# Kernel optimization log

Hardware: AMD Instinct MI355X
Metric: run time of the kernel (lower is better)

## Reference

```python
import jax, jax.numpy as jnp
import numpy as np

C_S, C_P, C_H, H, P_QK, P_V = 384, 128, 16, 12, 4, 8
B, N = 1, 512
INF = 1e5
EPS = 1e-8


def quat_to_rot(q):
    w, x, y, z = q[..., 0], q[..., 1], q[..., 2], q[..., 3]
    return jnp.stack([
        jnp.stack([1 - 2 * (y * y + z * z), 2 * (x * y - w * z), 2 * (x * z + w * y)], -1),
        jnp.stack([2 * (x * y + w * z), 1 - 2 * (x * x + z * z), 2 * (y * z - w * x)], -1),
        jnp.stack([2 * (x * z - w * y), 2 * (y * z + w * x), 1 - 2 * (x * x + y * y)], -1),
    ], -2)


def layer_norm(x, g, b):
    m = x.mean(-1, keepdims=True)
    v = ((x - m) ** 2).mean(-1, keepdims=True)
    return (x - m) * jax.lax.rsqrt(v + 1e-5) * g + b


def setup_inputs():
    key = jax.random.key(0)
    ks = iter(jax.random.split(key, 64))

    def w(shape, scale=0.02):
        return jax.random.normal(next(ks), shape, dtype=jnp.float32) * scale

    inp = {}
    inp['s'] = jax.random.normal(next(ks), (B, N, C_S), dtype=jnp.float32)
    inp['p'] = jax.random.normal(next(ks), (B, N, N, C_P), dtype=jnp.float32)
    q = jax.random.normal(next(ks), (B, N, 4), dtype=jnp.float32)
    inp['rot'] = quat_to_rot(q / jnp.linalg.norm(q, axis=-1, keepdims=True))
    inp['trans'] = jax.random.normal(next(ks), (B, N, 3), dtype=jnp.float32)
    inp['mask'] = jnp.ones((B, N), dtype=jnp.float32)
    inp['w_q'] = w((C_S, H * C_H)); inp['b_q'] = jnp.zeros((H * C_H,), jnp.float32)
    inp['w_kv'] = w((C_S, 2 * H * C_H)); inp['b_kv'] = jnp.zeros((2 * H * C_H,), jnp.float32)
    inp['w_qp'] = w((C_S, H * P_QK * 3)); inp['b_qp'] = jnp.zeros((H * P_QK * 3,), jnp.float32)
    inp['w_kvp'] = w((C_S, H * (P_QK + P_V) * 3)); inp['b_kvp'] = jnp.zeros((H * (P_QK + P_V) * 3,), jnp.float32)
    inp['w_b'] = w((C_P, H)); inp['b_b'] = jnp.zeros((H,), jnp.float32)
    inp['head_w'] = w((H,), 0.5)
    d_out = H * (C_H + C_P + P_V * 4)  # 2112
    inp['w_o'] = w((d_out, C_S)); inp['b_o'] = jnp.zeros((C_S,), jnp.float32)
    inp['ln1_g'] = jnp.ones((C_S,), jnp.float32); inp['ln1_b'] = jnp.zeros((C_S,), jnp.float32)
    for i in (1, 2, 3):
        inp['tw%d' % i] = w((C_S, C_S)); inp['tb%d' % i] = jnp.zeros((C_S,), jnp.float32)
    inp['ln2_g'] = jnp.ones((C_S,), jnp.float32); inp['ln2_b'] = jnp.zeros((C_S,), jnp.float32)
    inp['bb_w'] = w((C_S, 6)); inp['bb_b'] = jnp.zeros((6,), jnp.float32)
    return inp


def forward(s, p, rot, trans, mask, w_q, b_q, w_kv, b_kv, w_qp, b_qp, w_kvp, b_kvp,
            w_b, b_b, head_w, w_o, b_o, ln1_g, ln1_b,
            tw1, tb1, tw2, tb2, tw3, tb3, ln2_g, ln2_b, bb_w, bb_b):
    # ---- Invariant Point Attention ----
    q = (s @ w_q + b_q).reshape(B, N, H, C_H)
    k, v = jnp.split((s @ w_kv + b_kv).reshape(B, N, H, 2 * C_H), 2, axis=-1)
    qp = (s @ w_qp + b_qp).reshape(B, N, H * P_QK, 3)
    qp = (jnp.einsum('bnij,bnpj->bnpi', rot, qp) + trans[:, :, None, :]).reshape(B, N, H, P_QK, 3)
    kvp = (s @ w_kvp + b_kvp).reshape(B, N, H * (P_QK + P_V), 3)
    kvp = (jnp.einsum('bnij,bnpj->bnpi', rot, kvp) + trans[:, :, None, :]).reshape(B, N, H, P_QK + P_V, 3)
    kp, vp = kvp[..., :P_QK, :], kvp[..., P_QK:, :]
    bias = p @ w_b + b_b  # [B,N,N,H]
    a = jnp.einsum('bihc,bjhc->bhij', q, k) * float(np.sqrt(1.0 / (3 * C_H)))
    a = a + float(np.sqrt(1.0 / 3)) * jnp.transpose(bias, (0, 3, 1, 2))
    d2 = ((qp[:, :, None] - kp[:, None]) ** 2).sum(-1)  # [B,N,N,H,Pqk]
    hw = jax.nn.softplus(head_w) * float(np.sqrt(1.0 / (3 * (P_QK * 9.0 / 2))))
    pt_att = -0.5 * (d2 * hw[:, None]).sum(-1)  # [B,N,N,H]
    sq_mask = (mask[:, :, None] * mask[:, None, :] - 1.0) * INF  # [B,N,N]
    a = jax.nn.softmax(a + jnp.transpose(pt_att, (0, 3, 1, 2)) + sq_mask[:, None], axis=-1)
    o = jnp.einsum('bhij,bjhc->bihc', a, v).reshape(B, N, H * C_H)
    op = jnp.einsum('bhij,bjhpc->bihpc', a, vp) - trans[:, :, None, None, :]
    op = jnp.einsum('bnji,bnhpj->bnhpi', rot, op)  # invert-apply frames
    op_norm = jnp.sqrt((op ** 2).sum(-1) + EPS)  # [B,N,H,Pv]
    o_pair = jnp.einsum('bhij,bijc->bihc', a, p).reshape(B, N, H * C_P)
    cat = jnp.concatenate([o, op.reshape(B, N, H * P_V * 3), op_norm.reshape(B, N, H * P_V), o_pair], -1)
    s = s + cat @ w_o + b_o
    s = layer_norm(s, ln1_g, ln1_b)
    # ---- structure transition (1 layer, residual + LN) ----
    h = jax.nn.relu(s @ tw1 + tb1)
    h = jax.nn.relu(h @ tw2 + tb2)
    s = layer_norm(s + h @ tw3 + tb3, ln2_g, ln2_b)
    # ---- backbone update + frame compose ----
    upd = s @ bb_w + bb_b  # [B,N,6]
    quat = jnp.concatenate([jnp.ones((B, N, 1), s.dtype), upd[..., :3]], -1)
    quat = quat / jnp.linalg.norm(quat, axis=-1, keepdims=True)
    r_u = quat_to_rot(quat)
    rot_new = jnp.einsum('bnij,bnjk->bnik', rot, r_u)
    trans_new = jnp.einsum('bnij,bnj->bni', rot, upd[..., 3:]) + trans
    return s, rot_new, trans_new


def reference(s, p, rot, trans, mask, w_q, b_q, w_kv, b_kv, w_qp, b_qp, w_kvp, b_kvp,
              w_b, b_b, head_w, w_o, b_o, ln1_g, ln1_b,
              tw1, tb1, tw2, tb2, tw3, tb3, ln2_g, ln2_b, bb_w, bb_b):
    return forward(s, p, rot, trans, mask, w_q, b_q, w_kv, b_kv, w_qp, b_qp, w_kvp, b_kvp,
                   w_b, b_b, head_w, w_o, b_o, ln1_g, ln1_b,
                   tw1, tb1, tw2, tb2, tw3, tb3, ln2_g, ln2_b, bb_w, bb_b)
```

## Files before the change

kernel.cpp:

```cpp
#include <hip/hip_runtime.h>
#include <math.h>

#define N 512
#define CS 384
#define CP 128
#define CH 16
#define NH 12
#define NN (N*N)
#define DCAT 2112
#define INFV 100000.0f

__device__ __constant__ float SC_QK = 0.14433756729740643f;
#define SC_B  0.57735026918962576f
#define HW_SC 0.13608276348795434f

typedef __attribute__((ext_vector_type(8))) short bf16x8;
typedef __attribute__((ext_vector_type(4))) float f32x4;
typedef __attribute__((ext_vector_type(4))) short sh4;
typedef __attribute__((ext_vector_type(4))) unsigned u32x4;
typedef unsigned short ushort_t;

__device__ inline short f2bf(float v) {
    unsigned u = __builtin_bit_cast(unsigned, v);
    u += 0x7FFF + ((u >> 16) & 1);
    return (short)(u >> 16);
}
__device__ inline float bf2f(ushort_t u) {
    unsigned x = ((unsigned)u) << 16;
    return __builtin_bit_cast(float, x);
}
__device__ __forceinline__ unsigned cvtpk(float a, float b) {
    unsigned r;
    asm("v_cvt_pk_bf16_f32 %0, %1, %2" : "=v"(r) : "v"(a), "v"(b));
    return r;
}

__device__ __forceinline__ void gload16(const void* g, void* l) {
    __builtin_amdgcn_global_load_lds(
        (const __attribute__((address_space(1))) unsigned int*)g,
        (__attribute__((address_space(3))) unsigned int*)l,
        16, 0, 0);
}

struct PrepArgs {
    const float* wsrc0; const float* wsrc1; const float* wsrc2; const float* wsrc3;
    const float* wsrc4; const float* wsrc5; const float* wsrc6; const float* wsrc7;
    ushort_t* wdst0; ushort_t* wdst1; ushort_t* wdst2; ushort_t* wdst3;
    ushort_t* wdst4; ushort_t* wdst5; ushort_t* wdst6; ushort_t* wdst7;
    const float* s; ushort_t* sbf;
    const float* bq; const float* bkv; const float* bqp; const float* bkvp;
    float* biasp;
};

__global__ __launch_bounds__(256) void prep_kernel(PrepArgs a)
{
    const int b = blockIdx.x;
    if (b < 1668) {
        const float* src; ushort_t* dst; int begin, nx, Nc, K;
        if      (b < 72)   { src=a.wsrc0; dst=a.wdst0; begin=0;    nx=6;  Nc=192; K=384; }
        else if (b < 216)  { src=a.wsrc1; dst=a.wdst1; begin=72;   nx=12; Nc=384; K=384; }
        else if (b < 276)  { src=a.wsrc2; dst=a.wdst2; begin=216;  nx=5;  Nc=144; K=384; }
        else if (b < 444)  { src=a.wsrc3; dst=a.wdst3; begin=276;  nx=14; Nc=432; K=384; }
        else if (b < 1236) { src=a.wsrc4; dst=a.wdst4; begin=444;  nx=12; Nc=384; K=2112; }
        else if (b < 1380) { src=a.wsrc5; dst=a.wdst5; begin=1236; nx=12; Nc=384; K=384; }
        else if (b < 1524) { src=a.wsrc6; dst=a.wdst6; begin=1380; nx=12; Nc=384; K=384; }
        else               { src=a.wsrc7; dst=a.wdst7; begin=1524; nx=12; Nc=384; K=384; }
        int lb = b - begin;
        int cx = (lb % nx) * 32, ky = (lb / nx) * 32;
        __shared__ float tile[32][33];
        const int tx = threadIdx.x & 31, ty = threadIdx.x >> 5;
        for (int r = ty; r < 32; r += 8) {
            int c = cx + tx;
            tile[r][tx] = (c < Nc) ? src[(size_t)(ky + r) * Nc + c] : 0.f;
        }
        __syncthreads();
        for (int r = ty; r < 32; r += 8) {
            int orow = cx + r;
            if (orow < Nc)
                dst[(size_t)orow * K + ky + tx] = (ushort_t)f2bf(tile[tx][r]);
        }
    } else if (b < 1860) {
        int i4 = (b - 1668) * 256 + threadIdx.x;
        f32x4 v = *(const f32x4*)(a.s + (size_t)i4 * 4);
        sh4 o;
        o[0] = f2bf(v[0]); o[1] = f2bf(v[1]); o[2] = f2bf(v[2]); o[3] = f2bf(v[3]);
        *(sh4*)(a.sbf + (size_t)i4 * 4) = o;
    } else {
        for (int idx = threadIdx.x; idx < 1152; idx += 256) {
            float v;
            if (idx < 192)      v = a.bq[idx];
            else if (idx < 576) v = a.bkv[idx - 192];
            else if (idx < 720) v = a.bqp[idx - 576];
            else                v = a.bkvp[idx - 720];
            a.biasp[idx] = v;
        }
    }
}

__global__ __launch_bounds__(256) void gemm_bf16(
    const ushort_t* __restrict__ A, const ushort_t* __restrict__ Bt,
    float* __restrict__ part, int K, int KOUT, int nk)
{
    __shared__ __align__(16) ushort_t As[2][2048];
    __shared__ __align__(16) ushort_t Bs[2][2048];
    const int t = threadIdx.x, w = t >> 6, l = t & 63;
    const int i0 = blockIdx.x * 64, n0 = blockIdx.y * 64, sp = blockIdx.z;
    const int kbase = sp * nk * 32;

    const int srow = w * 16 + (l >> 2);
    const int skb = (l & 3) ^ ((srow >> 1) & 3);
    const ushort_t* aSrc = A + (size_t)(i0 + srow) * K + kbase + skb * 8;
    const ushort_t* bSrc = Bt + (size_t)(n0 + srow) * K + kbase + skb * 8;
    ushort_t* aDst = &As[0][0] + w * 512;
    ushort_t* bDst = &Bs[0][0] + w * 512;

    const int r0 = (w >> 1) * 32, c0 = (w & 1) * 32, lr = l & 15, hk = l >> 4;
    int aOff[2], bOff[2];
    #pragma unroll
    for (int m = 0; m < 2; ++m) {
        int row = r0 + m * 16 + lr;
        aOff[m] = row * 64 + ((hk ^ ((row >> 1) & 3)) << 4);
    }
    #pragma unroll
    for (int n = 0; n < 2; ++n) {
        int row = c0 + n * 16 + lr;
        bOff[n] = row * 64 + ((hk ^ ((row >> 1) & 3)) << 4);
    }

    f32x4 acc[2][2];
    #pragma unroll
    for (int m = 0; m < 2; ++m)
        #pragma unroll
        for (int n = 0; n < 2; ++n) acc[m][n] = (f32x4){0.f, 0.f, 0.f, 0.f};

    gload16(aSrc, aDst);
    gload16(bSrc, bDst);
    __syncthreads();

    int cur = 0;
    for (int it = 0; it < nk; ++it) {
        if (it + 1 < nk) {
            gload16(aSrc + (it + 1) * 32, aDst + (cur ^ 1) * 2048);
            gload16(bSrc + (it + 1) * 32, bDst + (cur ^ 1) * 2048);
        }
        const char* ab = (const char*)&As[cur][0];
        const char* bb = (const char*)&Bs[cur][0];
        bf16x8 a0 = *(const bf16x8*)(ab + aOff[0]);
        bf16x8 a1 = *(const bf16x8*)(ab + aOff[1]);
        bf16x8 b0 = *(const bf16x8*)(bb + bOff[0]);
        bf16x8 b1 = *(const bf16x8*)(bb + bOff[1]);
        acc[0][0] = __builtin_amdgcn_mfma_f32_16x16x32_bf16(a0, b0, acc[0][0], 0, 0, 0);
        acc[0][1] = __builtin_amdgcn_mfma_f32_16x16x32_bf16(a0, b1, acc[0][1], 0, 0, 0);
        acc[1][0] = __builtin_amdgcn_mfma_f32_16x16x32_bf16(a1, b0, acc[1][0], 0, 0, 0);
        acc[1][1] = __builtin_amdgcn_mfma_f32_16x16x32_bf16(a1, b1, acc[1][1], 0, 0, 0);
        __syncthreads();
        cur ^= 1;
    }

    #pragma unroll
    for (int m = 0; m < 2; ++m)
        #pragma unroll
        for (int n = 0; n < 2; ++n) {
            int col = n0 + c0 + n * 16 + lr;
            int rowb = i0 + r0 + m * 16 + (l >> 4) * 4;
            float* pr = part + ((size_t)sp * 512 + rowb) * KOUT + col;
            #pragma unroll
            for (int j = 0; j < 4; ++j)
                pr[(size_t)j * KOUT] = acc[m][n][j];
        }
}

__global__ void reduce_k(const float* __restrict__ parts, int S, int KOUT,
                         const float* __restrict__ bias, const float* __restrict__ resid,
                         int relu, float* __restrict__ outf, ushort_t* __restrict__ outbf)
{
    int i4 = blockIdx.x * 256 + threadIdx.x;
    int tot = 512 * KOUT / 4;
    if (i4 >= tot) return;
    int idx = i4 * 4, c = idx % KOUT;
    f32x4 v = *(const f32x4*)(bias + c);
    for (int s2 = 0; s2 < S; ++s2)
        v += *(const f32x4*)(parts + (size_t)s2 * 512 * KOUT + idx);
    if (resid) v += *(const f32x4*)(resid + idx);
    if (relu) {
        v[0] = fmaxf(v[0], 0.f); v[1] = fmaxf(v[1], 0.f);
        v[2] = fmaxf(v[2], 0.f); v[3] = fmaxf(v[3], 0.f);
    }
    if (outf) *(f32x4*)(outf + idx) = v;
    if (outbf) {
        sh4 o;
        o[0] = f2bf(v[0]); o[1] = f2bf(v[1]); o[2] = f2bf(v[2]); o[3] = f2bf(v[3]);
        *(sh4*)(outbf + idx) = o;
    }
}

__global__ void reduce_ln(const float* __restrict__ parts, int S,
                          const float* __restrict__ gbias, const float* __restrict__ resid,
                          const float* __restrict__ g, const float* __restrict__ b,
                          float* __restrict__ outf, ushort_t* __restrict__ outbf,
                          const float* __restrict__ bb_w, const float* __restrict__ bb_b,
                          const float* __restrict__ rot, const float* __restrict__ trans,
                          float* __restrict__ out_rot, float* __restrict__ out_trans)
{
    __shared__ float buf[384];
    __shared__ float red[2], red2[2];
    __shared__ float ush[2][6];
    const int i = blockIdx.x, t = threadIdx.x;
    float s = 0.f, sq = 0.f;
    for (int k = t; k < 384; k += 128) {
        float v = gbias[k] + resid[(size_t)i * 384 + k];
        for (int s2 = 0; s2 < S; ++s2)
            v += parts[((size_t)s2 * 512 + i) * 384 + k];
        buf[k] = v; s += v; sq += v * v;
    }
    for (int off = 32; off; off >>= 1) { s += __shfl_xor(s, off); sq += __shfl_xor(sq, off); }
    if ((t & 63) == 0) { red[t >> 6] = s; red2[t >> 6] = sq; }
    __syncthreads();
    float mean = (red[0] + red[1]) * (1.0f / 384.0f);
    float var = (red2[0] + red2[1]) * (1.0f / 384.0f) - mean * mean;
    float rstd = rsqrtf(var + 1e-5f);
    float onorm[3];
    #pragma unroll
    for (int kk = 0; kk < 3; ++kk) {
        int k = t + kk * 128;
        float o = (buf[k] - mean) * rstd * g[k] + b[k];
        onorm[kk] = o;
        if (outf) outf[(size_t)i * 384 + k] = o;
        if (outbf) outbf[(size_t)i * 384 + k] = (ushort_t)f2bf(o);
    }
    if (!bb_w) return;
    float u[6] = {0.f, 0.f, 0.f, 0.f, 0.f, 0.f};
    #pragma unroll
    for (int kk = 0; kk < 3; ++kk) {
        int k = t + kk * 128;
        float sv = onorm[kk];
        #pragma unroll
        for (int c = 0; c < 6; ++c) u[c] += sv * bb_w[k * 6 + c];
    }
    #pragma unroll
    for (int c = 0; c < 6; ++c)
        for (int off = 32; off; off >>= 1) u[c] += __shfl_xor(u[c], off);
    if ((t & 63) == 0) {
        #pragma unroll
        for (int c = 0; c < 6; ++c) ush[t >> 6][c] = u[c];
    }
    __syncthreads();
    if (t == 0) {
        float uu[6];
        #pragma unroll
        for (int c = 0; c < 6; ++c) uu[c] = ush[0][c] + ush[1][c] + bb_b[c];
        float inq = rsqrtf(1.0f + uu[0]*uu[0] + uu[1]*uu[1] + uu[2]*uu[2]);
        float w = inq, x = uu[0]*inq, y = uu[1]*inq, z = uu[2]*inq;
        float Ru[9];
        Ru[0] = 1.f - 2.f*(y*y + z*z); Ru[1] = 2.f*(x*y - w*z); Ru[2] = 2.f*(x*z + w*y);
        Ru[3] = 2.f*(x*y + w*z); Ru[4] = 1.f - 2.f*(x*x + z*z); Ru[5] = 2.f*(y*z - w*x);
        Ru[6] = 2.f*(x*z - w*y); Ru[7] = 2.f*(y*z + w*x); Ru[8] = 1.f - 2.f*(x*x + y*y);
        const float* R = rot + i * 9;
        #pragma unroll
        for (int a = 0; a < 3; ++a) {
            #pragma unroll
            for (int cc = 0; cc < 3; ++cc)
                out_rot[i * 9 + a * 3 + cc] =
                    R[a*3+0]*Ru[0+cc] + R[a*3+1]*Ru[3+cc] + R[a*3+2]*Ru[6+cc];
            out_trans[i * 3 + a] = R[a*3+0]*uu[3] + R[a*3+1]*uu[4] + R[a*3+2]*uu[5]
                                   + trans[i * 3 + a];
        }
    }
}

__global__ __launch_bounds__(256) void postproj_kernel(
    const float* __restrict__ parts, const float* __restrict__ biasp,
    const float* __restrict__ rot, const float* __restrict__ trans,
    const float* __restrict__ head_w, const float* __restrict__ mask,
    ushort_t* __restrict__ Qext, ushort_t* __restrict__ Kext, ushort_t* __restrict__ Vext)
{
    __shared__ float buf[1152];
    __shared__ float hwv[12], kc28[12];
    const int j = blockIdx.x, t = threadIdx.x;
    for (int c = t; c < 1152; c += 256)
        buf[c] = biasp[c] + parts[(size_t)j * 1152 + c] + parts[(size_t)(512 + j) * 1152 + c];
    if (t >= 192 && t < 204) {
        int h = t - 192;
        hwv[h] = HW_SC * log1pf(expf(head_w[h]));
    }
    __syncthreads();
    if (t < 192) {
        int base = 576 + t * 3;
        const float* R = rot + j * 9;
        const float* T = trans + j * 3;
        float x = buf[base], y = buf[base + 1], z = buf[base + 2];
        float nx = R[0]*x + R[1]*y + R[2]*z + T[0];
        float ny = R[3]*x + R[4]*y + R[5]*z + T[1];
        float nz = R[6]*x + R[7]*y + R[8]*z + T[2];
        buf[base] = nx; buf[base + 1] = ny; buf[base + 2] = nz;
    }
    __syncthreads();
    if (t < 12) {
        float s2 = 0.f;
        #pragma unroll
        for (int e = 0; e < 12; ++e) { float v = buf[720 + t * 36 + e]; s2 += v * v; }
        kc28[t] = -0.5f * hwv[t] * s2 + (mask[j] - 1.0f) * INFV;
    }
    __syncthreads();
    if (t < 192) {
        int h = t >> 4, c0 = (t & 15) * 2;
        float hwf = hwv[h];
        #pragma unroll
        for (int e = 0; e < 2; ++e) {
            int c = c0 + e;
            float qv, kv2;
            if (c < 16)      { qv = SC_QK * buf[h * 16 + c];           kv2 = buf[192 + h * 32 + c]; }
            else if (c < 28) { qv = hwf * buf[576 + h * 12 + (c - 16)]; kv2 = buf[720 + h * 36 + (c - 16)]; }
            else if (c == 28){ qv = 1.f;                               kv2 = kc28[h]; }
            else             { qv = 0.f;                               kv2 = 0.f; }
            Qext[(size_t)h * 16384 + j * 32 + c] = (ushort_t)f2bf(qv);
            Kext[(size_t)h * 16384 + j * 32 + c] = (ushort_t)f2bf(kv2);
        }
    }
    for (int idx = t; idx < 576; idx += 256) {
        int h = idx / 48, c = idx % 48;
        float v;
        if (c < 16)      v = buf[192 + h * 32 + 16 + c];
        else if (c < 40) v = buf[720 + h * 36 + 12 + (c - 16)];
        else             v = 0.f;
        Vext[(size_t)h * 24576 + c * 512 + j] = (ushort_t)f2bf(v);
    }
}

__global__ __launch_bounds__(256) void bias_mfma(
    const float* __restrict__ p, const float* __restrict__ w_b,
    const float* __restrict__ b_b, ushort_t* __restrict__ bias_b)
{
    __shared__ __align__(16) float Pf[64 * 128];
    __shared__ __align__(16) ushort_t Wbs[16 * 128];
    const int t = threadIdx.x, w = t >> 6;
    const size_t row0 = (size_t)blockIdx.x * 64;

    for (int idx = t; idx < 2048; idx += 256) {
        int h = idx >> 7, c = idx & 127;
        float v = (h < 12) ? w_b[c * 12 + h] : 0.f;
        int byte = h * 256 + ((c * 2) ^ ((h & 7) << 4));
        *(ushort_t*)((char*)Wbs + byte) = (ushort_t)f2bf(v);
    }
    #pragma unroll
    for (int k = 0; k < 8; ++k) {
        int s = k * 256 + t;
        int row = s >> 5, ch = s & 31;
        const char* src = (const char*)(p + (row0 + row) * 128) + ((ch ^ (row & 7)) * 16);
        gload16(src, (char*)Pf + (size_t)(k * 256 + w * 64) * 16);
    }
    __syncthreads();

    const int l = t & 63, lr = l & 15, hk = l >> 4;
    const int jb = w * 16;
    f32x4 acc = (f32x4){0.f, 0.f, 0.f, 0.f};
    #pragma unroll
    for (int ks = 0; ks < 4; ++ks) {
        int row = jb + lr;
        int kc = ks * 8 + hk * 2;
        const char* base = (const char*)Pf + row * 512;
        f32x4 v0 = *(const f32x4*)(base + ((kc ^ (row & 7)) * 16));
        f32x4 v1 = *(const f32x4*)(base + (((kc + 1) ^ (row & 7)) * 16));
        bf16x8 afr;
        afr[0] = f2bf(v0[0]); afr[1] = f2bf(v0[1]); afr[2] = f2bf(v0[2]); afr[3] = f2bf(v0[3]);
        afr[4] = f2bf(v1[0]); afr[5] = f2bf(v1[1]); afr[6] = f2bf(v1[2]); afr[7] = f2bf(v1[3]);
        bf16x8 bfr = *(const bf16x8*)((char*)Wbs + lr * 256 +
                        ((ks * 64 + hk * 16) ^ ((lr & 7) << 4)));
        acc = __builtin_amdgcn_mfma_f32_16x16x32_bf16(afr, bfr, acc, 0, 0, 0);
    }
    if (lr < 12) {
        float bb = b_b[lr];
        size_t gj = row0 + jb + hk * 4;
        sh4 o;
        #pragma unroll
        for (int r = 0; r < 4; ++r) o[r] = f2bf(SC_B * (acc[r] + bb));
        *(sh4*)(bias_b + (size_t)lr * NN + gj) = o;
    }
}

__global__ __launch_bounds__(256) void attn_mfma(
    const ushort_t* __restrict__ Qext, const ushort_t* __restrict__ Kext,
    const ushort_t* __restrict__ bias_b, const ushort_t* __restrict__ Vext,
    const float* __restrict__ rot, const float* __restrict__ trans,
    ushort_t* __restrict__ attn_b, ushort_t* __restrict__ catb)
{
    __shared__ float sc[16 * 516];
    __shared__ float redm[64];
    __shared__ float invr[16];
    __shared__ float opl[16][25];
    const int t = threadIdx.x, w = t >> 6, l = t & 63;
    const int i0 = blockIdx.x * 16, h = blockIdx.y;
    const int lr = l & 15, hk = l >> 4;

    #pragma unroll
    for (int it = 0; it < 8; ++it) {
        int elem = (t + it * 256) * 4;
        int i = elem >> 9, j = elem & 511;
        sh4 raw = *(const sh4*)(bias_b + (size_t)h * NN + (size_t)(i0 + i) * 512 + j);
        f32x4 v;
        v[0] = bf2f((ushort_t)raw[0]); v[1] = bf2f((ushort_t)raw[1]);
        v[2] = bf2f((ushort_t)raw[2]); v[3] = bf2f((ushort_t)raw[3]);
        *(f32x4*)(sc + i * 516 + j) = v;
    }
    __syncthreads();

    bf16x8 a0 = *(const bf16x8*)(Qext + (size_t)h * 16384 + (i0 + lr) * 32 + hk * 8);
    f32x4 acc[8];
    #pragma unroll
    for (int n = 0; n < 8; ++n) {
        bf16x8 b = *(const bf16x8*)(Kext + (size_t)h * 16384 +
                                    (w * 128 + n * 16 + lr) * 32 + hk * 8);
        acc[n] = __builtin_amdgcn_mfma_f32_16x16x32_bf16(a0, b, (f32x4){0.f,0.f,0.f,0.f}, 0, 0, 0);
    }

    float rmax[4] = {-3.0e38f, -3.0e38f, -3.0e38f, -3.0e38f};
    #pragma unroll
    for (int n = 0; n < 8; ++n) {
        int col = w * 128 + n * 16 + lr;
        #pragma unroll
        for (int r = 0; r < 4; ++r) {
            int row = hk * 4 + r;
            float v = acc[n][r] + sc[row * 516 + col];
            sc[row * 516 + col] = v;
            rmax[r] = fmaxf(rmax[r], v);
        }
    }
    #pragma unroll
    for (int r = 0; r < 4; ++r) {
        float v = rmax[r];
        v = fmaxf(v, __shfl_xor(v, 1));
        v = fmaxf(v, __shfl_xor(v, 2));
        v = fmaxf(v, __shfl_xor(v, 4));
        v = fmaxf(v, __shfl_xor(v, 8));
        if (lr == 0) redm[w * 16 + hk * 4 + r] = v;
    }
    __syncthreads();

    {
        int row = t >> 4, g = t & 15;
        float mx = fmaxf(fmaxf(redm[row], redm[16 + row]),
                         fmaxf(redm[32 + row], redm[48 + row]));
        float sum = 0.f;
        float* sr = sc + row * 516;
        for (int c = g; c < 512; c += 16) {
            float e = expf(sr[c] - mx);
            sr[c] = e;
            sum += e;
        }
        sum += __shfl_xor(sum, 1);
        sum += __shfl_xor(sum, 2);
        sum += __shfl_xor(sum, 4);
        sum += __shfl_xor(sum, 8);
        if (g == 0) invr[row] = 1.0f / sum;
    }
    __syncthreads();

    #pragma unroll
    for (int it = 0; it < 8; ++it) {
        int elem = (t + it * 256) * 4;
        int i = elem >> 9, j = elem & 511;
        f32x4 v = *(const f32x4*)(sc + i * 516 + j);
        float iv = invr[i];
        sh4 o;
        o[0] = f2bf(v[0] * iv); o[1] = f2bf(v[1] * iv);
        o[2] = f2bf(v[2] * iv); o[3] = f2bf(v[3] * iv);
        *(sh4*)(attn_b + (size_t)h * NN + (size_t)(i0 + i) * 512 + j) = o;
    }

    f32x4 acc3[3];
    acc3[0] = (f32x4){0.f,0.f,0.f,0.f};
    acc3[1] = (f32x4){0.f,0.f,0.f,0.f};
    acc3[2] = (f32x4){0.f,0.f,0.f,0.f};
    const ushort_t* vbase = Vext + (size_t)h * 24576 + lr * 512 + hk * 8;
    #pragma unroll
    for (int kt = 0; kt < 16; ++kt) {
        const float* srow = sc + lr * 516 + kt * 32 + hk * 8;
        f32x4 x0 = *(const f32x4*)(srow);
        f32x4 x1 = *(const f32x4*)(srow + 4);
        u32x4 ap;
        ap[0] = cvtpk(x0[0], x0[1]); ap[1] = cvtpk(x0[2], x0[3]);
        ap[2] = cvtpk(x1[0], x1[1]); ap[3] = cvtpk(x1[2], x1[3]);
        bf16x8 af = __builtin_bit_cast(bf16x8, ap);
        #pragma unroll
        for (int n = 0; n < 3; ++n) {
            bf16x8 bf = *(const bf16x8*)(vbase + n * 16 * 512 + kt * 32);
            acc3[n] = __builtin_amdgcn_mfma_f32_16x16x32_bf16(af, bf, acc3[n], 0, 0, 0);
        }
    }
    #pragma unroll
    for (int n = 0; n < 3; ++n) {
        int c = n * 16 + lr;
        #pragma unroll
        for (int r = 0; r < 4; ++r) {
            int ri = hk * 4 + r;
            float val = acc3[n][r] * invr[ri];
            if (c < 16)
                catb[(size_t)(i0 + ri) * DCAT + h * 16 + c] = (ushort_t)f2bf(val);
            else if (c < 40)
                opl[ri][c - 16] = val;
        }
    }
    __syncthreads();
    if (t < 128) {
        int i16 = t >> 3, pv = t & 7;
        int i = i0 + i16;
        const float* T = trans + i * 3;
        const float* R = rot + i * 9;
        float x = opl[i16][pv * 3 + 0] - T[0];
        float y = opl[i16][pv * 3 + 1] - T[1];
        float z = opl[i16][pv * 3 + 2] - T[2];
        float rx = R[0] * x + R[3] * y + R[6] * z;
        float ry = R[1] * x + R[4] * y + R[7] * z;
        float rz = R[2] * x + R[5] * y + R[8] * z;
        float nm = sqrtf(rx * rx + ry * ry + rz * rz + 1e-8f);
        ushort_t* cr = catb + (size_t)i * DCAT;
        cr[192 + h * 24 + pv * 3 + 0] = (ushort_t)f2bf(rx);
        cr[192 + h * 24 + pv * 3 + 1] = (ushort_t)f2bf(ry);
        cr[192 + h * 24 + pv * 3 + 2] = (ushort_t)f2bf(rz);
        cr[480 + h * 8 + pv] = (ushort_t)f2bf(nm);
    }
}

__global__ __launch_bounds__(256) void opair_mfma(
    const ushort_t* __restrict__ attn_b, const float* __restrict__ p,
    ushort_t* __restrict__ catb)
{
    __shared__ __align__(16) ushort_t As2[16 * 512];
    __shared__ __align__(16) ushort_t Pt[2][128 * 72];
    const int t = threadIdx.x, i = blockIdx.x;
    const int w = t >> 6, l = t & 63;
    const int lr = l & 15, hk = l >> 4;

    #pragma unroll
    for (int ii = 0; ii < 4; ++ii) {
        int idx = (t + ii * 256) * 8;
        int h = idx >> 9, j = idx & 511;
        bf16x8 v;
        if (h < 12) v = *(const bf16x8*)(attn_b + (size_t)h * NN + (size_t)i * 512 + j);
        else        v = (bf16x8){0,0,0,0,0,0,0,0};
        *(bf16x8*)((char*)As2 + h * 1024 + ((j * 2) ^ ((h & 7) << 4))) = v;
    }

    const int jA = (t >> 3) * 2;
    const int c0 = (t & 7) * 16;
    const float* psrc = p + (size_t)i * 65536;

    f32x4 va[4], vb[4];
    #pragma unroll
    for (int q = 0; q < 4; ++q) {
        va[q] = *(const f32x4*)(psrc + (size_t)jA * 128 + c0 + q * 4);
        vb[q] = *(const f32x4*)(psrc + (size_t)(jA + 1) * 128 + c0 + q * 4);
    }

    #define PACK_TILE(buf)                                                       \
        {                                                                        \
            ushort_t* ptw = &Pt[buf][0];                                         \
            _Pragma("unroll")                                                    \
            for (int e = 0; e < 16; ++e) {                                       \
                int c = c0 + e;                                                  \
                unsigned pk = cvtpk(va[e >> 2][e & 3], vb[e >> 2][e & 3]);       \
                int byte = c * 144 + ((jA * 2) ^ (((c >> 4) & 7) << 4));         \
                *(unsigned*)((char*)ptw + byte) = pk;                            \
            }                                                                    \
        }
    #define LOAD_TILE(tile)                                                      \
        {                                                                        \
            const float* s0 = psrc + (size_t)((tile) * 64 + jA) * 128 + c0;      \
            _Pragma("unroll")                                                    \
            for (int q = 0; q < 4; ++q) {                                        \
                va[q] = *(const f32x4*)(s0 + q * 4);                             \
                vb[q] = *(const f32x4*)(s0 + 128 + q * 4);                       \
            }                                                                    \
        }

    PACK_TILE(0);
    LOAD_TILE(1);

    f32x4 acc[2];
    acc[0] = (f32x4){0.f, 0.f, 0.f, 0.f};
    acc[1] = (f32x4){0.f, 0.f, 0.f, 0.f};

    int cur = 0;
    for (int tile = 0; tile < 8; ++tile) {
        __syncthreads();
        const char* pt = (const char*)&Pt[cur][0];
        #pragma unroll
        for (int ks = 0; ks < 2; ++ks) {
            bf16x8 afr = *(const bf16x8*)((char*)As2 + lr * 1024 +
                            ((tile * 128 + ks * 64 + hk * 16) ^ ((lr & 7) << 4)));
            #pragma unroll
            for (int n = 0; n < 2; ++n) {
                int c = w * 32 + n * 16 + lr;
                bf16x8 bfr = *(const bf16x8*)(pt + c * 144 +
                                ((ks * 64 + hk * 16) ^ (((c >> 4) & 7) << 4)));
                acc[n] = __builtin_amdgcn_mfma_f32_16x16x32_bf16(afr, bfr, acc[n], 0, 0, 0);
            }
        }
        if (tile < 7) {
            PACK_TILE(cur ^ 1);
            if (tile < 6) LOAD_TILE(tile + 2);
            cur ^= 1;
        }
    }
    #undef PACK_TILE
    #undef LOAD_TILE
    #pragma unroll
    for (int n = 0; n < 2; ++n) {
        int c = w * 32 + n * 16 + lr;
        #pragma unroll
        for (int r = 0; r < 4; ++r) {
            int h = hk * 4 + r;
            if (h < 12)
                catb[(size_t)i * DCAT + 576 + h * 128 + c] = (ushort_t)f2bf(acc[n][r]);
        }
    }
}

extern "C" void kernel_launch(void* const* d_in, const int* in_sizes, int n_in,
                              void* d_out, int out_size, void* d_ws, size_t ws_size,
                              hipStream_t stream)
{
    const float* s      = (const float*)d_in[0];
    const float* p      = (const float*)d_in[1];
    const float* rot    = (const float*)d_in[2];
    const float* trans  = (const float*)d_in[3];
    const float* mask   = (const float*)d_in[4];
    const float* w_q    = (const float*)d_in[5];
    const float* b_q    = (const float*)d_in[6];
    const float* w_kv   = (const float*)d_in[7];
    const float* b_kv   = (const float*)d_in[8];
    const float* w_qp   = (const float*)d_in[9];
    const float* b_qp   = (const float*)d_in[10];
    const float* w_kvp  = (const float*)d_in[11];
    const float* b_kvp  = (const float*)d_in[12];
    const float* w_b    = (const float*)d_in[13];
    const float* b_b    = (const float*)d_in[14];
    const float* head_w = (const float*)d_in[15];
    const float* w_o    = (const float*)d_in[16];
    const float* b_o    = (const float*)d_in[17];
    const float* ln1_g  = (const float*)d_in[18];
    const float* ln1_b  = (const float*)d_in[19];
    const float* tw1    = (const float*)d_in[20];
    const float* tb1    = (const float*)d_in[21];
    const float* tw2    = (const float*)d_in[22];
    const float* tb2    = (const float*)d_in[23];
    const float* tw3    = (const float*)d_in[24];
    const float* tb3    = (const float*)d_in[25];
    const float* ln2_g  = (const float*)d_in[26];
    const float* ln2_b  = (const float*)d_in[27];
    const float* bb_w   = (const float*)d_in[28];
    const float* bb_b   = (const float*)d_in[29];

    float* ws = (float*)d_ws;
    float*    parts = ws;
    float*    s1    = parts + 1179648;
    float*    biasp = s1 + 196608;
    ushort_t* ub     = (ushort_t*)(biasp + 1152);
    ushort_t* bias_b = ub;
    ushort_t* attn_b = bias_b + 3145728;
    ushort_t* catb   = attn_b + 3145728;
    ushort_t* sbf    = catb + 1081344;
    ushort_t* s1bf   = sbf + 196608;
    ushort_t* h1bf   = s1bf + 196608;
    ushort_t* h2bf   = h1bf + 196608;
    ushort_t* Qext   = h2bf + 196608;
    ushort_t* Kext   = Qext + 196608;
    ushort_t* Vext   = Kext + 196608;
    ushort_t* Wtp    = Vext + 294912;
    ushort_t* Wto    = Wtp + 442368;
    ushort_t* Wt1    = Wto + 811008;
    ushort_t* Wt2    = Wt1 + 147456;
    ushort_t* Wt3    = Wt2 + 147456;

    float* out_s     = (float*)d_out;
    float* out_rot   = out_s + 196608;
    float* out_trans = out_rot + 4608;

    PrepArgs pa;
    pa.wsrc0 = w_q;  pa.wdst0 = Wtp;
    pa.wsrc1 = w_kv; pa.wdst1 = Wtp + (size_t)192 * 384;
    pa.wsrc2 = w_qp; pa.wdst2 = Wtp + (size_t)576 * 384;
    pa.wsrc3 = w_kvp; pa.wdst3 = Wtp + (size_t)720 * 384;
    pa.wsrc4 = w_o;  pa.wdst4 = Wto;
    pa.wsrc5 = tw1;  pa.wdst5 = Wt1;
    pa.wsrc6 = tw2;  pa.wdst6 = Wt2;
    pa.wsrc7 = tw3;  pa.wdst7 = Wt3;
    pa.s = s; pa.sbf = sbf;
    pa.bq = b_q; pa.bkv = b_kv; pa.bqp = b_qp; pa.bkvp = b_kvp;
    pa.biasp = biasp;
    prep_kernel<<<1861, 256, 0, stream>>>(pa);

    gemm_bf16<<<dim3(8, 18, 2), 256, 0, stream>>>(sbf, Wtp, parts, 384, 1152, 6);
    postproj_kernel<<<512, 256, 0, stream>>>(parts, biasp, rot, trans, head_w, mask,
                                             Qext, Kext, Vext);

    bias_mfma<<<4096, 256, 0, stream>>>(p, w_b, b_b, bias_b);
    attn_mfma<<<dim3(32, 12), 256, 0, stream>>>(Qext, Kext, bias_b, Vext, rot, trans,
                                                attn_b, catb);
    opair_mfma<<<512, 256, 0, stream>>>(attn_b, p, catb);

    gemm_bf16<<<dim3(8, 6, 6), 256, 0, stream>>>(catb, Wto, parts, 2112, 384, 11);
    reduce_ln<<<512, 128, 0, stream>>>(parts, 6, b_o, s, ln1_g, ln1_b, s1, s1bf,
                                       nullptr, nullptr, nullptr, nullptr, nullptr, nullptr);

    gemm_bf16<<<dim3(8, 6, 3), 256, 0, stream>>>(s1bf, Wt1, parts, 384, 384, 4);
    reduce_k<<<192, 256, 0, stream>>>(parts, 3, 384, tb1, nullptr, 1, nullptr, h1bf);
    gemm_bf16<<<dim3(8, 6, 3), 256, 0, stream>>>(h1bf, Wt2, parts, 384, 384, 4);
    reduce_k<<<192, 256, 0, stream>>>(parts, 3, 384, tb2, nullptr, 1, nullptr, h2bf);
    gemm_bf16<<<dim3(8, 6, 3), 256, 0, stream>>>(h2bf, Wt3, parts, 384, 384, 4);
    reduce_ln<<<512, 128, 0, stream>>>(parts, 3, tb3, s1, ln2_g, ln2_b, out_s, nullptr,
                                       bb_w, bb_b, rot, trans, out_rot, out_trans);
}
```

Measured before the change: 129.1 us.

## Merge pair-bias projection into prep kernel and fuse split-K reduce into next GEMM

The pair-bias MFMA projection (4096 blocks) is folded into the prep kernel, which becomes one front kernel, so weight transposes and the bias projection share a single launch. The two reduce_k launches in the transition MLP are removed. Each next GEMM now sums the three split-K partials, adds the bias, applies ReLU and converts to bf16 while loading its A operand. Partials ping-pong between two workspace regions. This cuts three kernel launches and the intermediate bf16 round trips, but each GEMM block now reads fp32 partials redundantly across its N-tiles.

```diff
diff --git a/kernel.cpp b/kernel.cpp
--- a/kernel.cpp
+++ b/kernel.cpp
@@ -42,7 +42,7 @@
         16, 0, 0);
 }
 
-struct PrepArgs {
+struct FrontArgs {
     const float* wsrc0; const float* wsrc1; const float* wsrc2; const float* wsrc3;
     const float* wsrc4; const float* wsrc5; const float* wsrc6; const float* wsrc7;
     ushort_t* wdst0; ushort_t* wdst1; ushort_t* wdst2; ushort_t* wdst3;
@@ -50,49 +50,101 @@
     const float* s; ushort_t* sbf;
     const float* bq; const float* bkv; const float* bqp; const float* bkvp;
     float* biasp;
+    const float* p; const float* w_b; const float* b_b; ushort_t* bias_b;
 };
 
-__global__ __launch_bounds__(256) void prep_kernel(PrepArgs a)
+__global__ __launch_bounds__(256) void front_kernel(FrontArgs a)
 {
+    __shared__ __align__(16) char SM[36864];
     const int b = blockIdx.x;
-    if (b < 1668) {
-        const float* src; ushort_t* dst; int begin, nx, Nc, K;
-        if      (b < 72)   { src=a.wsrc0; dst=a.wdst0; begin=0;    nx=6;  Nc=192; K=384; }
-        else if (b < 216)  { src=a.wsrc1; dst=a.wdst1; begin=72;   nx=12; Nc=384; K=384; }
-        else if (b < 276)  { src=a.wsrc2; dst=a.wdst2; begin=216;  nx=5;  Nc=144; K=384; }
-        else if (b < 444)  { src=a.wsrc3; dst=a.wdst3; begin=276;  nx=14; Nc=432; K=384; }
-        else if (b < 1236) { src=a.wsrc4; dst=a.wdst4; begin=444;  nx=12; Nc=384; K=2112; }
-        else if (b < 1380) { src=a.wsrc5; dst=a.wdst5; begin=1236; nx=12; Nc=384; K=384; }
-        else if (b < 1524) { src=a.wsrc6; dst=a.wdst6; begin=1380; nx=12; Nc=384; K=384; }
-        else               { src=a.wsrc7; dst=a.wdst7; begin=1524; nx=12; Nc=384; K=384; }
-        int lb = b - begin;
-        int cx = (lb % nx) * 32, ky = (lb / nx) * 32;
-        __shared__ float tile[32][33];
-        const int tx = threadIdx.x & 31, ty = threadIdx.x >> 5;
-        for (int r = ty; r < 32; r += 8) {
-            int c = cx + tx;
-            tile[r][tx] = (c < Nc) ? src[(size_t)(ky + r) * Nc + c] : 0.f;
+    const int t = threadIdx.x;
+    if (b < 4096) {
+        float* Pf = (float*)SM;
+        ushort_t* Wbs = (ushort_t*)(SM + 32768);
+        const int w = t >> 6;
+        const size_t row0 = (size_t)b * 64;
+
+        for (int idx = t; idx < 2048; idx += 256) {
+            int h = idx >> 7, c = idx & 127;
+            float v = (h < 12) ? a.w_b[c * 12 + h] : 0.f;
+            int byte = h * 256 + ((c * 2) ^ ((h & 7) << 4));
+            *(ushort_t*)((char*)Wbs + byte) = (ushort_t)f2bf(v);
+        }
+        #pragma unroll
+        for (int k = 0; k < 8; ++k) {
+            int s2 = k * 256 + t;
+            int row = s2 >> 5, ch = s2 & 31;
+            const char* src = (const char*)(a.p + (row0 + row) * 128) + ((ch ^ (row & 7)) * 16);
+            gload16(src, (char*)Pf + (size_t)(k * 256 + w * 64) * 16);
         }
         __syncthreads();
-        for (int r = ty; r < 32; r += 8) {
-            int orow = cx + r;
-            if (orow < Nc)
-                dst[(size_t)orow * K + ky + tx] = (ushort_t)f2bf(tile[tx][r]);
-        }
-    } else if (b < 1860) {
-        int i4 = (b - 1668) * 256 + threadIdx.x;
-        f32x4 v = *(const f32x4*)(a.s + (size_t)i4 * 4);
-        sh4 o;
-        o[0] = f2bf(v[0]); o[1] = f2bf(v[1]); o[2] = f2bf(v[2]); o[3] = f2bf(v[3]);
-        *(sh4*)(a.sbf + (size_t)i4 * 4) = o;
+
+        const int l = t & 63, lr = l & 15, hk = l >> 4;
+        const int jb = w * 16;
+        f32x4 acc = (f32x4){0.f, 0.f, 0.f, 0.f};
+        #pragma unroll
+        for (int ks = 0; ks < 4; ++ks) {
+            int row = jb + lr;
+            int kc = ks * 8 + hk * 2;
+            const char* base = (const char*)Pf + row * 512;
+            f32x4 v0 = *(const f32x4*)(base + ((kc ^ (row & 7)) * 16));
+            f32x4 v1 = *(const f32x4*)(base + (((kc + 1) ^ (row & 7)) * 16));
+            bf16x8 afr;
+            afr[0] = f2bf(v0[0]); afr[1] = f2bf(v0[1]); afr[2] = f2bf(v0[2]); afr[3] = f2bf(v0[3]);
+            afr[4] = f2bf(v1[0]); afr[5] = f2bf(v1[1]); afr[6] = f2bf(v1[2]); afr[7] = f2bf(v1[3]);
+            bf16x8 bfr = *(const bf16x8*)((char*)Wbs + lr * 256 +
+                            ((ks * 64 + hk * 16) ^ ((lr & 7) << 4)));
+            acc = __builtin_amdgcn_mfma_f32_16x16x32_bf16(afr, bfr, acc, 0, 0, 0);
+        }
+        if (lr < 12) {
+            float bb = a.b_b[lr];
+            size_t gj = row0 + jb + hk * 4;
+            sh4 o;
+            #pragma unroll
+            for (int r = 0; r < 4; ++r) o[r] = f2bf(SC_B * (acc[r] + bb));
+            *(sh4*)(a.bias_b + (size_t)lr * NN + gj) = o;
+        }
     } else {
-        for (int idx = threadIdx.x; idx < 1152; idx += 256) {
-            float v;
-            if (idx < 192)      v = a.bq[idx];
-            else if (idx < 576) v = a.bkv[idx - 192];
-            else if (idx < 720) v = a.bqp[idx - 576];
-            else                v = a.bkvp[idx - 720];
-            a.biasp[idx] = v;
+        const int bp = b - 4096;
+        if (bp < 1668) {
+            const float* src; ushort_t* dst; int begin, nx, Nc, K;
+            if      (bp < 72)   { src=a.wsrc0; dst=a.wdst0; begin=0;    nx=6;  Nc=192; K=384; }
+            else if (bp < 216)  { src=a.wsrc1; dst=a.wdst1; begin=72;   nx=12; Nc=384; K=384; }
+            else if (bp < 276)  { src=a.wsrc2; dst=a.wdst2; begin=216;  nx=5;  Nc=144; K=384; }
+            else if (bp < 444)  { src=a.wsrc3; dst=a.wdst3; begin=276;  nx=14; Nc=432; K=384; }
+            else if (bp < 1236) { src=a.wsrc4; dst=a.wdst4; begin=444;  nx=12; Nc=384; K=2112; }
+            else if (bp < 1380) { src=a.wsrc5; dst=a.wdst5; begin=1236; nx=12; Nc=384; K=384; }
+            else if (bp < 1524) { src=a.wsrc6; dst=a.wdst6; begin=1380; nx=12; Nc=384; K=384; }
+            else                { src=a.wsrc7; dst=a.wdst7; begin=1524; nx=12; Nc=384; K=384; }
+            int lb = bp - begin;
+            int cx = (lb % nx) * 32, ky = (lb / nx) * 32;
+            float (*tile)[33] = (float(*)[33])SM;
+            const int tx = t & 31, ty = t >> 5;
+            for (int r = ty; r < 32; r += 8) {
+                int c = cx + tx;
+                tile[r][tx] = (c < Nc) ? src[(size_t)(ky + r) * Nc + c] : 0.f;
+            }
+            __syncthreads();
+            for (int r = ty; r < 32; r += 8) {
+                int orow = cx + r;
+                if (orow < Nc)
+                    dst[(size_t)orow * K + ky + tx] = (ushort_t)f2bf(tile[tx][r]);
+            }
+        } else if (bp < 1860) {
+            int i4 = (bp - 1668) * 256 + t;
+            f32x4 v = *(const f32x4*)(a.s + (size_t)i4 * 4);
+            sh4 o;
+            o[0] = f2bf(v[0]); o[1] = f2bf(v[1]); o[2] = f2bf(v[2]); o[3] = f2bf(v[3]);
+            *(sh4*)(a.sbf + (size_t)i4 * 4) = o;
+        } else {
+            for (int idx = t; idx < 1152; idx += 256) {
+                float v;
+                if (idx < 192)      v = a.bq[idx];
+                else if (idx < 576) v = a.bkv[idx - 192];
+                else if (idx < 720) v = a.bqp[idx - 576];
+                else                v = a.bkvp[idx - 720];
+                a.biasp[idx] = v;
+            }
         }
     }
 }
@@ -170,28 +222,107 @@
         }
 }
 
-__global__ void reduce_k(const float* __restrict__ parts, int S, int KOUT,
-                         const float* __restrict__ bias, const float* __restrict__ resid,
-                         int relu, float* __restrict__ outf, ushort_t* __restrict__ outbf)
+__global__ __launch_bounds__(256) void gemm_red(
+    const float* __restrict__ partsIn, const float* __restrict__ kbias,
+    const ushort_t* __restrict__ Bt, float* __restrict__ partOut, int nk)
 {
-    int i4 = blockIdx.x * 256 + threadIdx.x;
-    int tot = 512 * KOUT / 4;
-    if (i4 >= tot) return;
-    int idx = i4 * 4, c = idx % KOUT;
-    f32x4 v = *(const f32x4*)(bias + c);
-    for (int s2 = 0; s2 < S; ++s2)
-        v += *(const f32x4*)(parts + (size_t)s2 * 512 * KOUT + idx);
-    if (resid) v += *(const f32x4*)(resid + idx);
-    if (relu) {
-        v[0] = fmaxf(v[0], 0.f); v[1] = fmaxf(v[1], 0.f);
-        v[2] = fmaxf(v[2], 0.f); v[3] = fmaxf(v[3], 0.f);
-    }
-    if (outf) *(f32x4*)(outf + idx) = v;
-    if (outbf) {
-        sh4 o;
-        o[0] = f2bf(v[0]); o[1] = f2bf(v[1]); o[2] = f2bf(v[2]); o[3] = f2bf(v[3]);
-        *(sh4*)(outbf + idx) = o;
-    }
+    __shared__ __align__(16) ushort_t As[2][2048];
+    __shared__ __align__(16) ushort_t Bs[2][2048];
+    const int t = threadIdx.x, w = t >> 6, l = t & 63;
+    const int i0 = blockIdx.x * 64, n0 = blockIdx.y * 64, sp = blockIdx.z;
+    const int kbase = sp * nk * 32;
+
+    const int srow = w * 16 + (l >> 2);
+    const int skb = (l & 3) ^ ((srow >> 1) & 3);
+    const ushort_t* bSrc = Bt + (size_t)(n0 + srow) * 384 + kbase + skb * 8;
+    ushort_t* bDst = &Bs[0][0] + w * 512;
+
+    const int ar = t >> 2, apch = t & 3;
+    const int agch = apch ^ ((ar >> 1) & 3);
+    const float* aBase = partsIn + (size_t)(i0 + ar) * 384 + kbase + agch * 8;
+    const int aByte = ar * 64 + apch * 16;
+
+    const int r0 = (w >> 1) * 32, c0 = (w & 1) * 32, lr = l & 15, hk = l >> 4;
+    int aOff[2], bOff[2];
+    #pragma unroll
+    for (int m = 0; m < 2; ++m) {
+        int row = r0 + m * 16 + lr;
+        aOff[m] = row * 64 + ((hk ^ ((row >> 1) & 3)) << 4);
+    }
+    #pragma unroll
+    for (int n = 0; n < 2; ++n) {
+        int row = c0 + n * 16 + lr;
+        bOff[n] = row * 64 + ((hk ^ ((row >> 1) & 3)) << 4);
+    }
+
+    f32x4 av0, av1;
+    #define A_LOAD(it)                                                            \
+        {                                                                         \
+            const float* ap = aBase + (it) * 32;                                  \
+            av0 = *(const f32x4*)(ap) + *(const f32x4*)(ap + 196608)              \
+                + *(const f32x4*)(ap + 393216);                                   \
+            av1 = *(const f32x4*)(ap + 4) + *(const f32x4*)(ap + 196608 + 4)      \
+                + *(const f32x4*)(ap + 393216 + 4);                               \
+        }
+    #define A_STORE(buf, it)                                                      \
+        {                                                                         \
+            int kk = kbase + (it) * 32 + agch * 8;                                \
+            f32x4 kb0 = *(const f32x4*)(kbias + kk);                              \
+            f32x4 kb1 = *(const f32x4*)(kbias + kk + 4);                          \
+            f32x4 s0 = av0 + kb0, s1 = av1 + kb1;                                 \
+            u32x4 pk;                                                             \
+            pk[0] = cvtpk(fmaxf(s0[0], 0.f), fmaxf(s0[1], 0.f));                  \
+            pk[1] = cvtpk(fmaxf(s0[2], 0.f), fmaxf(s0[3], 0.f));                  \
+            pk[2] = cvtpk(fmaxf(s1[0], 0.f), fmaxf(s1[1], 0.f));                  \
+            pk[3] = cvtpk(fmaxf(s1[2], 0.f), fmaxf(s1[3], 0.f));                  \
+            *(u32x4*)((char*)&As[buf][0] + aByte) = pk;                           \
+        }
+
+    f32x4 acc[2][2];
+    #pragma unroll
+    for (int m = 0; m < 2; ++m)
+        #pragma unroll
+        for (int n = 0; n < 2; ++n) acc[m][n] = (f32x4){0.f, 0.f, 0.f, 0.f};
+
+    gload16(bSrc, bDst);
+    A_LOAD(0);
+    A_STORE(0, 0);
+    __syncthreads();
+
+    int cur = 0;
+    for (int it = 0; it < nk; ++it) {
+        if (it + 1 < nk) {
+            gload16(bSrc + (it + 1) * 32, bDst + (cur ^ 1) * 2048);
+            A_LOAD(it + 1);
+        }
+        const char* ab = (const char*)&As[cur][0];
+        const char* bb = (const char*)&Bs[cur][0];
+        bf16x8 a0 = *(const bf16x8*)(ab + aOff[0]);
+        bf16x8 a1 = *(const bf16x8*)(ab + aOff[1]);
+        bf16x8 b0 = *(const bf16x8*)(bb + bOff[0]);
+        bf16x8 b1 = *(const bf16x8*)(bb + bOff[1]);
+        acc[0][0] = __builtin_amdgcn_mfma_f32_16x16x32_bf16(a0, b0, acc[0][0], 0, 0, 0);
+        acc[0][1] = __builtin_amdgcn_mfma_f32_16x16x32_bf16(a0, b1, acc[0][1], 0, 0, 0);
+        acc[1][0] = __builtin_amdgcn_mfma_f32_16x16x32_bf16(a1, b0, acc[1][0], 0, 0, 0);
+        acc[1][1] = __builtin_amdgcn_mfma_f32_16x16x32_bf16(a1, b1, acc[1][1], 0, 0, 0);
+        if (it + 1 < nk) A_STORE(cur ^ 1, it + 1);
+        __syncthreads();
+        cur ^= 1;
+    }
+    #undef A_LOAD
+    #undef A_STORE
+
+    #pragma unroll
+    for (int m = 0; m < 2; ++m)
+        #pragma unroll
+        for (int n = 0; n < 2; ++n) {
+            int col = n0 + c0 + n * 16 + lr;
+            int rowb = i0 + r0 + m * 16 + (l >> 4) * 4;
+            float* pr = partOut + ((size_t)sp * 512 + rowb) * 384 + col;
+            #pragma unroll
+            for (int j = 0; j < 4; ++j)
+                pr[(size_t)j * 384] = acc[m][n][j];
+        }
 }
 
 __global__ void reduce_ln(const float* __restrict__ parts, int S,
@@ -324,57 +455,6 @@
         else if (c < 40) v = buf[720 + h * 36 + 12 + (c - 16)];
         else             v = 0.f;
         Vext[(size_t)h * 24576 + c * 512 + j] = (ushort_t)f2bf(v);
-    }
-}
-
-__global__ __launch_bounds__(256) void bias_mfma(
-    const float* __restrict__ p, const float* __restrict__ w_b,
-    const float* __restrict__ b_b, ushort_t* __restrict__ bias_b)
-{
-    __shared__ __align__(16) float Pf[64 * 128];
-    __shared__ __align__(16) ushort_t Wbs[16 * 128];
-    const int t = threadIdx.x, w = t >> 6;
-    const size_t row0 = (size_t)blockIdx.x * 64;
-
-    for (int idx = t; idx < 2048; idx += 256) {
-        int h = idx >> 7, c = idx & 127;
-        float v = (h < 12) ? w_b[c * 12 + h] : 0.f;
-        int byte = h * 256 + ((c * 2) ^ ((h & 7) << 4));
-        *(ushort_t*)((char*)Wbs + byte) = (ushort_t)f2bf(v);
-    }
-    #pragma unroll
-    for (int k = 0; k < 8; ++k) {
-        int s = k * 256 + t;
-        int row = s >> 5, ch = s & 31;
-        const char* src = (const char*)(p + (row0 + row) * 128) + ((ch ^ (row & 7)) * 16);
-        gload16(src, (char*)Pf + (size_t)(k * 256 + w * 64) * 16);
-    }
-    __syncthreads();
-
-    const int l = t & 63, lr = l & 15, hk = l >> 4;
-    const int jb = w * 16;
-    f32x4 acc = (f32x4){0.f, 0.f, 0.f, 0.f};
-    #pragma unroll
-    for (int ks = 0; ks < 4; ++ks) {
-        int row = jb + lr;
-        int kc = ks * 8 + hk * 2;
-        const char* base = (const char*)Pf + row * 512;
-        f32x4 v0 = *(const f32x4*)(base + ((kc ^ (row & 7)) * 16));
-        f32x4 v1 = *(const f32x4*)(base + (((kc + 1) ^ (row & 7)) * 16));
-        bf16x8 afr;
-        afr[0] = f2bf(v0[0]); afr[1] = f2bf(v0[1]); afr[2] = f2bf(v0[2]); afr[3] = f2bf(v0[3]);
-        afr[4] = f2bf(v1[0]); afr[5] = f2bf(v1[1]); afr[6] = f2bf(v1[2]); afr[7] = f2bf(v1[3]);
-        bf16x8 bfr = *(const bf16x8*)((char*)Wbs + lr * 256 +
-                        ((ks * 64 + hk * 16) ^ ((lr & 7) << 4)));
-        acc = __builtin_amdgcn_mfma_f32_16x16x32_bf16(afr, bfr, acc, 0, 0, 0);
-    }
-    if (lr < 12) {
-        float bb = b_b[lr];
-        size_t gj = row0 + jb + hk * 4;
-        sh4 o;
-        #pragma unroll
-        for (int r = 0; r < 4; ++r) o[r] = f2bf(SC_B * (acc[r] + bb));
-        *(sh4*)(bias_b + (size_t)lr * NN + gj) = o;
     }
 }
 
@@ -652,9 +732,10 @@
     const float* bb_b   = (const float*)d_in[29];
 
     float* ws = (float*)d_ws;
-    float*    parts = ws;
-    float*    s1    = parts + 1179648;
-    float*    biasp = s1 + 196608;
+    float*    parts  = ws;
+    float*    partsB = parts + 589824;
+    float*    s1     = parts + 1179648;
+    float*    biasp  = s1 + 196608;
     ushort_t* ub     = (ushort_t*)(biasp + 1152);
     ushort_t* bias_b = ub;
     ushort_t* attn_b = bias_b + 3145728;
@@ -676,25 +757,25 @@
     float* out_rot   = out_s + 196608;
     float* out_trans = out_rot + 4608;
 
-    PrepArgs pa;
-    pa.wsrc0 = w_q;  pa.wdst0 = Wtp;
-    pa.wsrc1 = w_kv; pa.wdst1 = Wtp + (size_t)192 * 384;
-    pa.wsrc2 = w_qp; pa.wdst2 = Wtp + (size_t)576 * 384;
-    pa.wsrc3 = w_kvp; pa.wdst3 = Wtp + (size_t)720 * 384;
-    pa.wsrc4 = w_o;  pa.wdst4 = Wto;
-    pa.wsrc5 = tw1;  pa.wdst5 = Wt1;
-    pa.wsrc6 = tw2;  pa.wdst6 = Wt2;
-    pa.wsrc7 = tw3;  pa.wdst7 = Wt3;
-    pa.s = s; pa.sbf = sbf;
-    pa.bq = b_q; pa.bkv = b_kv; pa.bqp = b_qp; pa.bkvp = b_kvp;
-    pa.biasp = biasp;
-    prep_kernel<<<1861, 256, 0, stream>>>(pa);
+    FrontArgs fa;
+    fa.wsrc0 = w_q;  fa.wdst0 = Wtp;
+    fa.wsrc1 = w_kv; fa.wdst1 = Wtp + (size_t)192 * 384;
+    fa.wsrc2 = w_qp; fa.wdst2 = Wtp + (size_t)576 * 384;
+    fa.wsrc3 = w_kvp; fa.wdst3 = Wtp + (size_t)720 * 384;
+    fa.wsrc4 = w_o;  fa.wdst4 = Wto;
+    fa.wsrc5 = tw1;  fa.wdst5 = Wt1;
+    fa.wsrc6 = tw2;  fa.wdst6 = Wt2;
+    fa.wsrc7 = tw3;  fa.wdst7 = Wt3;
+    fa.s = s; fa.sbf = sbf;
+    fa.bq = b_q; fa.bkv = b_kv; fa.bqp = b_qp; fa.bkvp = b_kvp;
+    fa.biasp = biasp;
+    fa.p = p; fa.w_b = w_b; fa.b_b = b_b; fa.bias_b = bias_b;
+    front_kernel<<<5957, 256, 0, stream>>>(fa);
 
     gemm_bf16<<<dim3(8, 18, 2), 256, 0, stream>>>(sbf, Wtp, parts, 384, 1152, 6);
     postproj_kernel<<<512, 256, 0, stream>>>(parts, biasp, rot, trans, head_w, mask,
                                              Qext, Kext, Vext);
 
-    bias_mfma<<<4096, 256, 0, stream>>>(p, w_b, b_b, bias_b);
     attn_mfma<<<dim3(32, 12), 256, 0, stream>>>(Qext, Kext, bias_b, Vext, rot, trans,
                                                 attn_b, catb);
     opair_mfma<<<512, 256, 0, stream>>>(attn_b, p, catb);
@@ -704,10 +785,8 @@
                                        nullptr, nullptr, nullptr, nullptr, nullptr, nullptr);
 
     gemm_bf16<<<dim3(8, 6, 3), 256, 0, stream>>>(s1bf, Wt1, parts, 384, 384, 4);
-    reduce_k<<<192, 256, 0, stream>>>(parts, 3, 384, tb1, nullptr, 1, nullptr, h1bf);
-    gemm_bf16<<<dim3(8, 6, 3), 256, 0, stream>>>(h1bf, Wt2, parts, 384, 384, 4);
-    reduce_k<<<192, 256, 0, stream>>>(parts, 3, 384, tb2, nullptr, 1, nullptr, h2bf);
-    gemm_bf16<<<dim3(8, 6, 3), 256, 0, stream>>>(h2bf, Wt3, parts, 384, 384, 4);
+    gemm_red<<<dim3(8, 6, 3), 256, 0, stream>>>(parts, tb1, Wt2, partsB, 4);
+    gemm_red<<<dim3(8, 6, 3), 256, 0, stream>>>(partsB, tb2, Wt3, parts, 4);
     reduce_ln<<<512, 128, 0, stream>>>(parts, 3, tb3, s1, ln2_g, ln2_b, out_s, nullptr,
                                        bb_w, bb_b, rot, trans, out_rot, out_trans);
 }
```

New measurement: 124.7 us, median of 2. 1.04x faster.
